# Performance work log

Measured on AMD Instinct MI355X. Metric: run time of the kernel, lower is better.

## Reference

```python
import jax, jax.numpy as jnp
import numpy as np

# Lloyd-Max (Max 1960) optimal 16-level quantizer for N(0,1), bits=4
_CODEBOOK_4 = np.array([-2.7326, -2.069, -1.6181, -1.2562, -0.9424, -0.6568,
                        -0.3881, -0.1284, 0.1284, 0.3881, 0.6568, 0.9424,
                        1.2562, 1.6181, 2.069, 2.7326], dtype=np.float32)
DIM = 256


def setup_inputs() -> dict:
    key = jax.random.key(0)
    kx, kq = jax.random.split(key)
    x = jax.random.normal(kx, (4, 4096, DIM), dtype=jnp.float32)
    # orthogonal rotation via QR of a Gaussian matrix (mirrors torch.linalg.qr)
    rotation, _ = jnp.linalg.qr(jax.random.normal(kq, (DIM, DIM), dtype=jnp.float32))
    codebook = jnp.asarray(_CODEBOOK_4)
    return {"x": x, "rotation": rotation, "codebook": codebook}


def reference(x, rotation, codebook):
    shape = x.shape
    d = shape[-1]
    sqrt_d = jnp.sqrt(jnp.asarray(d, dtype=x.dtype))
    x_flat = x.reshape(-1, d)                                   # (N, d)
    x_norm = jnp.maximum(
        jnp.linalg.norm(x_flat, axis=-1, keepdims=True), 1e-8)  # (N, 1)
    u = x_flat / x_norm                                         # unit vectors
    y_scaled = (u @ rotation.T) * sqrt_d                        # ~N(0,1) coords
    # nearest codebook entry per scalar coordinate: (N, d, K) -> argmin over K
    idx = jnp.argmin(jnp.abs(y_scaled[..., None] - codebook), axis=-1)
    y_hat = codebook[idx] / sqrt_d                              # (N, d)
    x_hat = (y_hat @ rotation) * x_norm                         # de-rotate, rescale
    return x_hat.reshape(shape)
```

## Files before the change

### kernel.cpp

```cpp
#include <hip/hip_runtime.h>

typedef _Float16 f16;
typedef _Float16 f16x4 __attribute__((ext_vector_type(4)));
typedef _Float16 f16x8 __attribute__((ext_vector_type(8)));
typedef float f32x16 __attribute__((ext_vector_type(16)));
typedef float f32x4 __attribute__((ext_vector_type(4)));

#define APITCH 264
#define WREG 67584

__global__ __launch_bounds__(512) void prep_kernel(const float* __restrict__ R,
                                                   f16* __restrict__ ws) {
  __shared__ float Lrs[32][260];
  const int b = blockIdx.x;
  const int g = b >> 2, h = b & 3;
  const int t = threadIdx.x;
  f16* W1h = ws;
  f16* W1l = ws + WREG;
  f16* W2h = ws + 2 * WREG;

  #pragma unroll
  for (int it = 0; it < 4; ++it) {
    int c = it * 512 + t;
    int row = c >> 6, c4 = (c & 63) * 4;
    f32x4 v = *(const f32x4*)&R[(long)(32 * g + row) * 256 + c4];
    *(f32x4*)&Lrs[row][c4] = v;
  }
  __syncthreads();

  if (t < 256) {
    int f_loc = 4 * h + (t >> 6), l = t & 63;
    int k0 = 16 * f_loc + 8 * (l >> 5);
    const float* src = &Lrs[l & 31][k0];
    f16x8 hi, lo;
    #pragma unroll
    for (int j = 0; j < 8; ++j) {
      float v = src[j] * 256.0f;
      f16 hh = (f16)v;
      hi[j] = hh;
      lo[j] = (f16)(v - (float)hh);
    }
    long o = (long)(g * 16 + f_loc) * 512 + l * 8;
    *(f16x8*)(W1h + o) = hi;
    *(f16x8*)(W1l + o) = lo;
  } else {
    int u = t - 256;
    int gp = 2 * h + (u >> 7), e = (u >> 6) & 1, l = u & 63;
    int lr0 = 16 * e + 8 * (l >> 5);
    int col = 32 * gp + (l & 31);
    f16x8 hv;
    #pragma unroll
    for (int j = 0; j < 8; ++j) hv[j] = (f16)Lrs[lr0 + j][col];
    long o = (long)(gp * 16 + 2 * g + e) * 512 + l * 8;
    *(f16x8*)(W2h + o) = hv;
  }
}

__global__ __launch_bounds__(512, 4) void tq_main(
    const float* __restrict__ X, const float* __restrict__ CB,
    const f16* __restrict__ ws, float* __restrict__ OUT) {
  __shared__ f16 A1h[32][APITCH];
  __shared__ f16 A1l[32][APITCH];
  __shared__ float s2s[32];

  const int tid = threadIdx.x;
  const int lane = tid & 63;
  const int wv = tid >> 6;
  const int lrow = lane & 31;
  const int kg = lane >> 5;
  const long row0 = (long)blockIdx.x * 32;

  const f16* W1h = ws;
  const f16* W1l = ws + WREG;
  const f16* W2h = ws + 2 * WREG;

  const int r = tid >> 4, q = tid & 15;
  const float* xp = X + (row0 + r) * 256 + q * 16;
  float xa[16];
  #pragma unroll
  for (int i = 0; i < 4; ++i) {
    f32x4 v = ((const f32x4*)xp)[i];
    xa[4 * i] = v.x; xa[4 * i + 1] = v.y; xa[4 * i + 2] = v.z; xa[4 * i + 3] = v.w;
  }

  float cbf[16];
  #pragma unroll
  for (int i = 0; i < 16; ++i) cbf[i] = CB[i];

  float ss = 0.f;
  #pragma unroll
  for (int i = 0; i < 16; ++i) ss += xa[i] * xa[i];
  ss += __shfl_xor(ss, 8, 16);
  ss += __shfl_xor(ss, 4, 16);
  ss += __shfl_xor(ss, 2, 16);
  ss += __shfl_xor(ss, 1, 16);
  float nrm = fmaxf(sqrtf(ss), 1e-8f);
  float s1f = 4096.0f / nrm;
  if (q == 0) s2s[r] = nrm * 0.0625f;

  #pragma unroll
  for (int c8 = 0; c8 < 2; ++c8) {
    f16x8 h, l;
    #pragma unroll
    for (int j = 0; j < 8; ++j) {
      float a = xa[c8 * 8 + j] * s1f;
      f16 hh = (f16)a;
      h[j] = hh;
      l[j] = (f16)(a - (float)hh);
    }
    *(f16x8*)&A1h[r][q * 16 + c8 * 8] = h;
    *(f16x8*)&A1l[r][q * 16 + c8 * 8] = l;
  }
  __syncthreads();

  const f16* W1hp = W1h + (long)(wv * 16) * 512 + lane * 8;
  const f16* W1lp = W1l + (long)(wv * 16) * 512 + lane * 8;
  f16x8 bh0 = *(const f16x8*)(W1hp);
  f16x8 bl0 = *(const f16x8*)(W1lp);
  f16x8 bh1 = *(const f16x8*)(W1hp + 512);
  f16x8 bl1 = *(const f16x8*)(W1lp + 512);

  f32x16 zv;
  #pragma unroll
  for (int i = 0; i < 16; ++i) zv[i] = 0.0f;
  f32x16 accH = zv, accL = zv;

  #pragma unroll
  for (int ks = 0; ks < 16; ks += 2) {
    {
      const int k0 = ks * 16 + kg * 8;
      f16x8 ah = *(const f16x8*)&A1h[lrow][k0];
      f16x8 al = *(const f16x8*)&A1l[lrow][k0];
      accH = __builtin_amdgcn_mfma_f32_32x32x16_f16(ah, bh0, accH, 0, 0, 0);
      accL = __builtin_amdgcn_mfma_f32_32x32x16_f16(al, bh0, accL, 0, 0, 0);
      accH = __builtin_amdgcn_mfma_f32_32x32x16_f16(ah, bl0, accH, 0, 0, 0);
      bh0 = *(const f16x8*)(W1hp + (ks + 2) * 512);
      bl0 = *(const f16x8*)(W1lp + (ks + 2) * 512);
    }
    {
      const int k0 = (ks + 1) * 16 + kg * 8;
      f16x8 ah = *(const f16x8*)&A1h[lrow][k0];
      f16x8 al = *(const f16x8*)&A1l[lrow][k0];
      accH = __builtin_amdgcn_mfma_f32_32x32x16_f16(ah, bh1, accH, 0, 0, 0);
      accL = __builtin_amdgcn_mfma_f32_32x32x16_f16(al, bh1, accL, 0, 0, 0);
      accH = __builtin_amdgcn_mfma_f32_32x32x16_f16(ah, bl1, accH, 0, 0, 0);
      bh1 = *(const f16x8*)(W1hp + (ks + 3) * 512);
      bl1 = *(const f16x8*)(W1lp + (ks + 3) * 512);
    }
  }

  const f16* W2p = W2h + (long)(wv * 16) * 512 + lane * 8;
  f16x8 c0 = *(const f16x8*)(W2p);
  f16x8 c1 = *(const f16x8*)(W2p + 512);
  f16x8 c2 = *(const f16x8*)(W2p + 1024);
  f16x8 c3 = *(const f16x8*)(W2p + 1536);

  float M[15];
  #pragma unroll
  for (int t = 0; t < 15; ++t) M[t] = 65536.0f * (0.5f * (cbf[t] + cbf[t + 1]));
  unsigned int cpk[8];
  #pragma unroll
  for (int i = 0; i < 8; ++i) {
    unsigned short lb = __builtin_bit_cast(unsigned short, (f16)cbf[2 * i]);
    unsigned short hb = __builtin_bit_cast(unsigned short, (f16)cbf[2 * i + 1]);
    cpk[i] = ((unsigned int)hb << 16) | (unsigned int)lb;
  }

  __syncthreads();

  f16 (*Qs)[APITCH] = A1h;
  #pragma unroll
  for (int rr = 0; rr < 16; ++rr) {
    float y = accH[rr] + accL[rr];
    int row = 4 * kg + (rr & 3) + 8 * (rr >> 2);
    int kk = 32 * wv + lrow;
    bool b3 = y > M[7];
    float m2 = b3 ? M[11] : M[3];
    bool b2 = y > m2;
    float m1 = b3 ? (b2 ? M[13] : M[9]) : (b2 ? M[5] : M[1]);
    bool b1 = y > m1;
    float m0 = b1 ? (b3 ? (b2 ? M[14] : M[10]) : (b2 ? M[6] : M[2]))
                  : (b3 ? (b2 ? M[12] : M[8]) : (b2 ? M[4] : M[0]));
    bool b0 = y > m0;
    unsigned int pp = b3 ? (b2 ? (b1 ? cpk[7] : cpk[6]) : (b1 ? cpk[5] : cpk[4]))
                         : (b2 ? (b1 ? cpk[3] : cpk[2]) : (b1 ? cpk[1] : cpk[0]));
    unsigned short qb = (unsigned short)(b0 ? (pp >> 16) : (pp & 0xFFFFu));
    Qs[row][kk] = __builtin_bit_cast(f16, qb);
  }
  __syncthreads();

  f32x16 acc2a = zv, acc2b = zv;
  #pragma unroll
  for (int ks = 0; ks < 16; ks += 4) {
    {
      f16x8 qa = *(const f16x8*)&Qs[lrow][ks * 16 + kg * 8];
      acc2a = __builtin_amdgcn_mfma_f32_32x32x16_f16(qa, c0, acc2a, 0, 0, 0);
      c0 = *(const f16x8*)(W2p + (ks + 4) * 512);
    }
    {
      f16x8 qa = *(const f16x8*)&Qs[lrow][(ks + 1) * 16 + kg * 8];
      acc2b = __builtin_amdgcn_mfma_f32_32x32x16_f16(qa, c1, acc2b, 0, 0, 0);
      c1 = *(const f16x8*)(W2p + (ks + 5) * 512);
    }
    {
      f16x8 qa = *(const f16x8*)&Qs[lrow][(ks + 2) * 16 + kg * 8];
      acc2a = __builtin_amdgcn_mfma_f32_32x32x16_f16(qa, c2, acc2a, 0, 0, 0);
      c2 = *(const f16x8*)(W2p + (ks + 6) * 512);
    }
    {
      f16x8 qa = *(const f16x8*)&Qs[lrow][(ks + 3) * 16 + kg * 8];
      acc2b = __builtin_amdgcn_mfma_f32_32x32x16_f16(qa, c3, acc2b, 0, 0, 0);
      c3 = *(const f16x8*)(W2p + (ks + 7) * 512);
    }
  }

  #pragma unroll
  for (int rr = 0; rr < 16; ++rr) {
    int row = 4 * kg + (rr & 3) + 8 * (rr >> 2);
    int col = 32 * wv + lrow;
    OUT[(row0 + row) * 256 + col] = (acc2a[rr] + acc2b[rr]) * s2s[row];
  }
}

#define FB_APITCH 264
#define FB_B1PITCH 40
#define FB_B2PITCH 264

__global__ __launch_bounds__(256, 1) void tq_main_fb(
    const float* __restrict__ X, const float* __restrict__ R,
    const float* __restrict__ CB, float* __restrict__ OUT) {
  __shared__ f16 A1h[64][FB_APITCH];
  __shared__ f16 A1l[64][FB_APITCH];
  __shared__ f16 Qs[64][FB_APITCH];
  __shared__ f32x4 Braw[2624];
  __shared__ float pn[4][64];
  __shared__ float s1s[64];
  __shared__ float s2s[64];

  f16 (*B1h)[FB_B1PITCH] = (f16(*)[FB_B1PITCH])Braw;
  f16 (*B1l)[FB_B1PITCH] = (f16(*)[FB_B1PITCH])((char*)Braw + 20480);
  f16 (*B2h)[FB_B2PITCH] = (f16(*)[FB_B2PITCH])Braw;

  const int tid = threadIdx.x;
  const int lane = tid & 63;
  const int wv = tid >> 6;
  const int lrow = lane & 31;
  const int kg = lane >> 5;
  const long row0 = (long)blockIdx.x * 64;

  float cbf[16];
  #pragma unroll
  for (int i = 0; i < 16; ++i) cbf[i] = CB[i];
  float M[15];
  #pragma unroll
  for (int t = 0; t < 15; ++t) M[t] = 65536.0f * (0.5f * (cbf[t] + cbf[t + 1]));
  unsigned int cpk[8];
  #pragma unroll
  for (int i = 0; i < 8; ++i) {
    unsigned short lb = __builtin_bit_cast(unsigned short, (f16)cbf[2 * i]);
    unsigned short hb = __builtin_bit_cast(unsigned short, (f16)cbf[2 * i + 1]);
    cpk[i] = ((unsigned int)hb << 16) | (unsigned int)lb;
  }

  const int xrow = tid >> 2, xq = tid & 3;
  const float* xp = X + (row0 + xrow) * 256 + xq * 64;
  float xa[64];
  #pragma unroll
  for (int i = 0; i < 16; ++i) {
    f32x4 v = ((const f32x4*)xp)[i];
    xa[4 * i] = v.x; xa[4 * i + 1] = v.y; xa[4 * i + 2] = v.z; xa[4 * i + 3] = v.w;
  }
  float ss = 0.f;
  #pragma unroll
  for (int i = 0; i < 64; ++i) ss += xa[i] * xa[i];
  pn[xq][xrow] = ss;
  __syncthreads();
  if (tid < 64) {
    float s = pn[0][tid] + pn[1][tid] + pn[2][tid] + pn[3][tid];
    float nrm = fmaxf(sqrtf(s), 1e-8f);
    s1s[tid] = 4096.0f / nrm;
    s2s[tid] = nrm * 0.0625f;
  }
  __syncthreads();

  {
    float s1f = s1s[xrow];
    #pragma unroll
    for (int c8 = 0; c8 < 8; ++c8) {
      f16x8 h, l;
      #pragma unroll
      for (int j = 0; j < 8; ++j) {
        float a = xa[c8 * 8 + j] * s1f;
        f16 hh = (f16)a;
        h[j] = hh;
        l[j] = (f16)(a - (float)hh);
      }
      *(f16x8*)&A1h[xrow][xq * 64 + c8 * 8] = h;
      *(f16x8*)&A1l[xrow][xq * 64 + c8 * 8] = l;
    }
  }

  f32x4 pf[8];
  #pragma unroll
  for (int q = 0; q < 8; ++q) {
    int c = q * 256 + tid;
    pf[q] = *(const f32x4*)&R[(long)(c >> 3) * 256 + ((c & 7) * 4)];
  }

  f32x16 zv;
  #pragma unroll
  for (int i = 0; i < 16; ++i) zv[i] = 0.0f;
  f32x16 acc[2][2];
  acc[0][0] = zv; acc[0][1] = zv; acc[1][0] = zv; acc[1][1] = zv;

  for (int kp = 0; kp < 8; ++kp) {
    __syncthreads();
    #pragma unroll
    for (int q = 0; q < 8; ++q) {
      int c = q * 256 + tid;
      int n = c >> 3, k4 = (c & 7) * 4;
      f16x4 h, l;
      #pragma unroll
      for (int j = 0; j < 4; ++j) {
        float sv = pf[q][j] * 256.0f;
        f16 hh = (f16)sv;
        h[j] = hh;
        l[j] = (f16)(sv - (float)hh);
      }
      *(f16x4*)&B1h[n][k4] = h;
      *(f16x4*)&B1l[n][k4] = l;
    }
    __syncthreads();
    if (kp < 7) {
      #pragma unroll
      for (int q = 0; q < 8; ++q) {
        int c = q * 256 + tid;
        pf[q] = *(const f32x4*)&R[(long)(c >> 3) * 256 + (kp + 1) * 32 + ((c & 7) * 4)];
      }
    }
    #pragma unroll
    for (int ks = 0; ks < 2; ++ks) {
      const int k0 = kp * 32 + ks * 16 + kg * 8;
      const int lk = ks * 16 + kg * 8;
      f16x8 ah[2], al[2], bhf[2], blf[2];
      #pragma unroll
      for (int m = 0; m < 2; ++m) {
        ah[m] = *(const f16x8*)&A1h[32 * m + lrow][k0];
        al[m] = *(const f16x8*)&A1l[32 * m + lrow][k0];
      }
      #pragma unroll
      for (int n = 0; n < 2; ++n) {
        int col = 64 * wv + 32 * n + lrow;
        bhf[n] = *(const f16x8*)&B1h[col][lk];
        blf[n] = *(const f16x8*)&B1l[col][lk];
      }
      #pragma unroll
      for (int m = 0; m < 2; ++m)
        #pragma unroll
        for (int n = 0; n < 2; ++n) {
          acc[m][n] = __builtin_amdgcn_mfma_f32_32x32x16_f16(ah[m], bhf[n], acc[m][n], 0, 0, 0);
          acc[m][n] = __builtin_amdgcn_mfma_f32_32x32x16_f16(al[m], bhf[n], acc[m][n], 0, 0, 0);
          acc[m][n] = __builtin_amdgcn_mfma_f32_32x32x16_f16(ah[m], blf[n], acc[m][n], 0, 0, 0);
          acc[m][n] = __builtin_amdgcn_mfma_f32_32x32x16_f16(al[m], blf[n], acc[m][n], 0, 0, 0);
        }
    }
  }

  #pragma unroll
  for (int q = 0; q < 8; ++q) {
    int c = q * 256 + tid;
    pf[q] = *(const f32x4*)&R[(long)(c >> 6) * 256 + ((c & 63) * 4)];
  }

  #pragma unroll
  for (int m = 0; m < 2; ++m)
    #pragma unroll
    for (int n = 0; n < 2; ++n)
      #pragma unroll
      for (int rr = 0; rr < 16; ++rr) {
        float y = acc[m][n][rr];
        int row = 32 * m + 4 * kg + (rr & 3) + 8 * (rr >> 2);
        int kk = 64 * wv + 32 * n + lrow;
        bool b3 = y > M[7];
        float m2 = b3 ? M[11] : M[3];
        bool b2 = y > m2;
        float m1 = b3 ? (b2 ? M[13] : M[9]) : (b2 ? M[5] : M[1]);
        bool b1 = y > m1;
        float m0 = b1 ? (b3 ? (b2 ? M[14] : M[10]) : (b2 ? M[6] : M[2]))
                      : (b3 ? (b2 ? M[12] : M[8]) : (b2 ? M[4] : M[0]));
        bool b0 = y > m0;
        unsigned int pp = b3 ? (b2 ? (b1 ? cpk[7] : cpk[6]) : (b1 ? cpk[5] : cpk[4]))
                             : (b2 ? (b1 ? cpk[3] : cpk[2]) : (b1 ? cpk[1] : cpk[0]));
        unsigned short qb = (unsigned short)(b0 ? (pp >> 16) : (pp & 0xFFFFu));
        Qs[row][kk] = __builtin_bit_cast(f16, qb);
      }
  __syncthreads();

  f32x16 acc2[2][2];
  acc2[0][0] = zv; acc2[0][1] = zv; acc2[1][0] = zv; acc2[1][1] = zv;

  for (int kp = 0; kp < 8; ++kp) {
    if (kp) __syncthreads();
    #pragma unroll
    for (int q = 0; q < 8; ++q) {
      int c = q * 256 + tid;
      int k = c >> 6, n4 = (c & 63) * 4;
      f16x4 h;
      #pragma unroll
      for (int j = 0; j < 4; ++j) h[j] = (f16)pf[q][j];
      *(f16x4*)&B2h[k][n4] = h;
    }
    __syncthreads();
    if (kp < 7) {
      #pragma unroll
      for (int q = 0; q < 8; ++q) {
        int c = q * 256 + tid;
        pf[q] = *(const f32x4*)&R[(long)((kp + 1) * 32 + (c >> 6)) * 256 + ((c & 63) * 4)];
      }
    }
    #pragma unroll
    for (int ks = 0; ks < 2; ++ks) {
      const int k0 = kp * 32 + ks * 16 + kg * 8;
      const int lk = ks * 16 + kg * 8;
      f16x8 qa[2], bb[2];
      #pragma unroll
      for (int m = 0; m < 2; ++m) qa[m] = *(const f16x8*)&Qs[32 * m + lrow][k0];
      #pragma unroll
      for (int n = 0; n < 2; ++n) {
        int colg = 64 * wv + 32 * n + lrow;
        #pragma unroll
        for (int j = 0; j < 8; ++j) bb[n][j] = B2h[lk + j][colg];
      }
      #pragma unroll
      for (int m = 0; m < 2; ++m)
        #pragma unroll
        for (int n = 0; n < 2; ++n)
          acc2[m][n] = __builtin_amdgcn_mfma_f32_32x32x16_f16(qa[m], bb[n], acc2[m][n], 0, 0, 0);
    }
  }

  #pragma unroll
  for (int m = 0; m < 2; ++m)
    #pragma unroll
    for (int n = 0; n < 2; ++n)
      #pragma unroll
      for (int rr = 0; rr < 16; ++rr) {
        int row = 32 * m + 4 * kg + (rr & 3) + 8 * (rr >> 2);
        int col = 64 * wv + 32 * n + lrow;
        OUT[(row0 + row) * 256 + col] = acc2[m][n][rr] * s2s[row];
      }
}

extern "C" void kernel_launch(void* const* d_in, const int* in_sizes, int n_in,
                              void* d_out, int out_size, void* d_ws, size_t ws_size,
                              hipStream_t stream) {
  const float* X = (const float*)d_in[0];
  const float* R = (const float*)d_in[1];
  const float* CB = (const float*)d_in[2];
  float* OUT = (float*)d_out;
  const int nrows = in_sizes[0] / 256;

  if (ws_size >= (size_t)3 * WREG * sizeof(f16)) {
    f16* ws = (f16*)d_ws;
    prep_kernel<<<32, 512, 0, stream>>>(R, ws);
    tq_main<<<nrows / 32, 512, 0, stream>>>(X, CB, ws, OUT);
  } else {
    tq_main_fb<<<nrows / 64, 256, 0, stream>>>(X, R, CB, OUT);
  }
}
```

Before: 26.12 us.

## Prefetch W1 fragments earlier and deeper, use separate Qs buffer to drop barrier

Issues the first four stages of W1 fragment loads before the X load and normalization, so global latency overlaps the preprocessing. The software pipeline depth in the first MFMA loop grows from two to four stages. A dedicated LDS buffer for the quantized tile replaces aliasing of A1h, which removes one __syncthreads. The cost is more registers and extra LDS per block, which can lower the number of resident blocks.

Result: faster. 25.40 us, median of 2 (-2.7%).

```diff
diff --git a/kernel.cpp b/kernel.cpp
--- a/kernel.cpp
+++ b/kernel.cpp
@@ -61,6 +61,7 @@
     const f16* __restrict__ ws, float* __restrict__ OUT) {
   __shared__ f16 A1h[32][APITCH];
   __shared__ f16 A1l[32][APITCH];
+  __shared__ f16 Qs[32][APITCH];
   __shared__ float s2s[32];
 
   const int tid = threadIdx.x;
@@ -82,6 +83,17 @@
     f32x4 v = ((const f32x4*)xp)[i];
     xa[4 * i] = v.x; xa[4 * i + 1] = v.y; xa[4 * i + 2] = v.z; xa[4 * i + 3] = v.w;
   }
+
+  const f16* W1hp = W1h + (long)(wv * 16) * 512 + lane * 8;
+  const f16* W1lp = W1l + (long)(wv * 16) * 512 + lane * 8;
+  f16x8 bh0 = *(const f16x8*)(W1hp);
+  f16x8 bl0 = *(const f16x8*)(W1lp);
+  f16x8 bh1 = *(const f16x8*)(W1hp + 512);
+  f16x8 bl1 = *(const f16x8*)(W1lp + 512);
+  f16x8 bh2 = *(const f16x8*)(W1hp + 1024);
+  f16x8 bl2 = *(const f16x8*)(W1lp + 1024);
+  f16x8 bh3 = *(const f16x8*)(W1hp + 1536);
+  f16x8 bl3 = *(const f16x8*)(W1lp + 1536);
 
   float cbf[16];
   #pragma unroll
@@ -113,41 +125,31 @@
   }
   __syncthreads();
 
-  const f16* W1hp = W1h + (long)(wv * 16) * 512 + lane * 8;
-  const f16* W1lp = W1l + (long)(wv * 16) * 512 + lane * 8;
-  f16x8 bh0 = *(const f16x8*)(W1hp);
-  f16x8 bl0 = *(const f16x8*)(W1lp);
-  f16x8 bh1 = *(const f16x8*)(W1hp + 512);
-  f16x8 bl1 = *(const f16x8*)(W1lp + 512);
-
   f32x16 zv;
   #pragma unroll
   for (int i = 0; i < 16; ++i) zv[i] = 0.0f;
   f32x16 accH = zv, accL = zv;
 
-  #pragma unroll
-  for (int ks = 0; ks < 16; ks += 2) {
-    {
-      const int k0 = ks * 16 + kg * 8;
-      f16x8 ah = *(const f16x8*)&A1h[lrow][k0];
-      f16x8 al = *(const f16x8*)&A1l[lrow][k0];
-      accH = __builtin_amdgcn_mfma_f32_32x32x16_f16(ah, bh0, accH, 0, 0, 0);
-      accL = __builtin_amdgcn_mfma_f32_32x32x16_f16(al, bh0, accL, 0, 0, 0);
-      accH = __builtin_amdgcn_mfma_f32_32x32x16_f16(ah, bl0, accH, 0, 0, 0);
-      bh0 = *(const f16x8*)(W1hp + (ks + 2) * 512);
-      bl0 = *(const f16x8*)(W1lp + (ks + 2) * 512);
-    }
-    {
-      const int k0 = (ks + 1) * 16 + kg * 8;
-      f16x8 ah = *(const f16x8*)&A1h[lrow][k0];
-      f16x8 al = *(const f16x8*)&A1l[lrow][k0];
-      accH = __builtin_amdgcn_mfma_f32_32x32x16_f16(ah, bh1, accH, 0, 0, 0);
-      accL = __builtin_amdgcn_mfma_f32_32x32x16_f16(al, bh1, accL, 0, 0, 0);
-      accH = __builtin_amdgcn_mfma_f32_32x32x16_f16(ah, bl1, accH, 0, 0, 0);
-      bh1 = *(const f16x8*)(W1hp + (ks + 3) * 512);
-      bl1 = *(const f16x8*)(W1lp + (ks + 3) * 512);
-    }
-  }
+#define MM1_STAGE(BH, BL, KS)                                                   \
+  {                                                                             \
+    const int k0 = (KS) * 16 + kg * 8;                                          \
+    f16x8 ah = *(const f16x8*)&A1h[lrow][k0];                                   \
+    f16x8 al = *(const f16x8*)&A1l[lrow][k0];                                   \
+    accH = __builtin_amdgcn_mfma_f32_32x32x16_f16(ah, BH, accH, 0, 0, 0);       \
+    accL = __builtin_amdgcn_mfma_f32_32x32x16_f16(al, BH, accL, 0, 0, 0);       \
+    accH = __builtin_amdgcn_mfma_f32_32x32x16_f16(ah, BL, accH, 0, 0, 0);       \
+    BH = *(const f16x8*)(W1hp + ((KS) + 4) * 512);                              \
+    BL = *(const f16x8*)(W1lp + ((KS) + 4) * 512);                              \
+  }
+
+  #pragma unroll
+  for (int ksb = 0; ksb < 16; ksb += 4) {
+    MM1_STAGE(bh0, bl0, ksb)
+    MM1_STAGE(bh1, bl1, ksb + 1)
+    MM1_STAGE(bh2, bl2, ksb + 2)
+    MM1_STAGE(bh3, bl3, ksb + 3)
+  }
+#undef MM1_STAGE
 
   const f16* W2p = W2h + (long)(wv * 16) * 512 + lane * 8;
   f16x8 c0 = *(const f16x8*)(W2p);
@@ -166,9 +168,6 @@
     cpk[i] = ((unsigned int)hb << 16) | (unsigned int)lb;
   }
 
-  __syncthreads();
-
-  f16 (*Qs)[APITCH] = A1h;
   #pragma unroll
   for (int rr = 0; rr < 16; ++rr) {
     float y = accH[rr] + accL[rr];
```
